# Performance work log

Measured on AMD Instinct MI355X. Metric: run time of the kernel, lower is better.

Reference implementation:

```python
import jax, jax.numpy as jnp
import numpy as np


def setup_inputs() -> dict:
    key = jax.random.key(0)
    kx, ky = jax.random.split(key)
    B, Sx, Sy, D = 8, 2048, 2048, 128
    x = jax.random.normal(kx, (B, Sx, D), dtype=jnp.float32)
    y = jax.random.normal(ky, (B, Sy, D), dtype=jnp.float32)
    return {"x": x, "y": y}


def reference(x, y):
    # score[b, i, j] = softmax_j(x[b,i,:] . y[b,j,:])
    score = jax.nn.softmax(jnp.einsum("bid,bjd->bij", x, y), axis=-1)
    # dropout is identity in eval mode (reference baseline)
    att_map = jnp.einsum("bij,bjd->bid", score, y)
    return x + att_map
```

## Files before the change

kernel.cpp:

```cpp
#include <hip/hip_runtime.h>
#include <hip/hip_fp16.h>


#define SX 2048
#define SY 2048
#define DD 128
#define KVBLK 64
#define NWAVE 8
#define QBLK (NWAVE * 32)
#define NTHREADS (NWAVE * 64)
#define L2E 1.4426950408889634f
#define RTHR 4.0f

typedef __attribute__((ext_vector_type(8))) _Float16 f16x8;
typedef __attribute__((ext_vector_type(4))) _Float16 f16x4;
typedef __attribute__((ext_vector_type(4))) float f32x4;
typedef __attribute__((ext_vector_type(16))) float f32x16;
typedef __attribute__((ext_vector_type(4))) unsigned int u32x4;

template<bool WRITEB>
__global__ __launch_bounds__(256) void prepass(const float* __restrict__ y,
                                               _Float16* __restrict__ yB,
                                               _Float16* __restrict__ yT)
{
    __shared__ _Float16 T[64 * 64];
    char* Tb = (char*)T;
    const int tid = (int)threadIdx.x;
    const int b = blockIdx.y;
    const int k0 = (blockIdx.x >> 1) * 64;
    const int d0 = (blockIdx.x & 1) * 64;
    const float* yb = y + (size_t)b * SY * DD;
#pragma unroll
    for (int t = 0; t < 2; ++t) {
        int cid = t * 256 + tid;
        int row = cid >> 3, c = cid & 7;
        const float* gp = yb + (size_t)(k0 + row) * DD + d0 + c * 8;
        f32x4 a0 = *(const f32x4*)gp;
        f32x4 a1 = *(const f32x4*)(gp + 4);
        f16x8 v;
#pragma unroll
        for (int j = 0; j < 4; ++j) { v[j] = (_Float16)a0[j]; v[4 + j] = (_Float16)a1[j]; }
        if constexpr (WRITEB)
            *(f16x8*)(yB + ((size_t)b * SY + k0 + row) * DD + d0 + c * 8) = v;
        *(f16x8*)(Tb + ((row * 128 + c * 16) ^ ((row & 7) << 4))) = v;
    }
    __syncthreads();
#pragma unroll
    for (int t = 0; t < 2; ++t) {
        int cid = t * 256 + tid;
        int drow = cid >> 3, ck = cid & 7;
        f16x8 v;
#pragma unroll
        for (int j = 0; j < 8; ++j)
            v[j] = *(const _Float16*)(Tb + ((((ck * 8 + j) * 128) + drow * 2) ^ (j << 4)));
        *(f16x8*)(yT + ((size_t)b * DD + d0 + drow) * SY + k0 + ck * 8) = v;
    }
}

template<bool SPLITOUT, int MODE>
__global__ __launch_bounds__(NTHREADS) void attn_fwd(
    const float* __restrict__ xg, const float* __restrict__ yg,
    const _Float16* __restrict__ yB, const _Float16* __restrict__ yT,
    float* __restrict__ og, _Float16* __restrict__ Opart,
    float* __restrict__ mpart, float* __restrict__ lpart,
    int kv_len, int nb)
{
    __shared__ __align__(16) unsigned char smem[2][32768];

    const int tid = (int)threadIdx.x;
    const int lane = tid & 63;
    const int wv = tid >> 6;
    const int l31 = lane & 31;
    const int hi = lane >> 5;
    const int swz = (l31 & 7) << 4;
    const int b = blockIdx.y;
    const int qbase = blockIdx.x * QBLK;
    const int sp = blockIdx.z;
    const int kv_begin = sp * kv_len;
    const int nt = kv_len / KVBLK;

    const float* xb = xg + (size_t)b * SX * DD;
    const float* yb = yg + (size_t)b * SY * DD;

    const int qrow = qbase + wv * 32 + l31;
    f16x8 qreg[8];
#pragma unroll
    for (int kst = 0; kst < 8; ++kst) {
        const float* qp = xb + (size_t)qrow * DD + kst * 16 + hi * 8;
        f32x4 q0 = *(const f32x4*)qp;
        f32x4 q1 = *(const f32x4*)(qp + 4);
        f16x8 v;
#pragma unroll
        for (int j = 0; j < 4; ++j) { v[j] = (_Float16)q0[j]; v[4 + j] = (_Float16)q1[j]; }
        qreg[kst] = v;
    }

    f16x8 kh[2];
    f32x4 kf[4];
    f16x8 vh[2];

    auto LOADT = [&](int kv0) {
#pragma unroll
        for (int c = 0; c < 2; ++c) {
            int cid = c * NTHREADS + tid;
            int krow = cid >> 4, kc8 = cid & 15;
            if constexpr (MODE == 2) {
                kh[c] = *(const f16x8*)(yB + ((size_t)b * SY + kv0 + krow) * DD + kc8 * 8);
            } else {
                const float* gp = yb + (size_t)(kv0 + krow) * DD + kc8 * 8;
                kf[c * 2]     = *(const f32x4*)gp;
                kf[c * 2 + 1] = *(const f32x4*)(gp + 4);
            }
        }
        if constexpr (MODE >= 1) {
#pragma unroll
            for (int c = 0; c < 2; ++c) {
                int cid = c * NTHREADS + tid;
                int d = cid >> 3, kc = cid & 7;
                vh[c] = *(const f16x8*)(yT + ((size_t)b * DD + d) * SY + kv0 + kc * 8);
            }
        }
    };
    auto STORET = [&](char* Kb, char* Vb) {
#pragma unroll
        for (int c = 0; c < 2; ++c) {
            int cid = c * NTHREADS + tid;
            int krow = cid >> 4, kc8 = cid & 15;
            f16x8 kv;
            if constexpr (MODE == 2) {
                kv = kh[c];
            } else {
#pragma unroll
                for (int j = 0; j < 4; ++j) { kv[j] = (_Float16)kf[c * 2][j]; kv[4 + j] = (_Float16)kf[c * 2 + 1][j]; }
            }
            *(f16x8*)(Kb + ((krow * 256 + kc8 * 16) ^ ((krow & 7) << 4))) = kv;
            if constexpr (MODE == 0) {
#pragma unroll
                for (int j = 0; j < 8; ++j) {
                    int d = kc8 * 8 + j;
                    *(_Float16*)(Vb + ((d * 128 + krow * 2) ^ ((d & 7) << 4))) = kv[j];
                }
            }
        }
        if constexpr (MODE >= 1) {
#pragma unroll
            for (int c = 0; c < 2; ++c) {
                int cid = c * NTHREADS + tid;
                int d = cid >> 3, kc = cid & 7;
                *(f16x8*)(Vb + ((d * 128 + kc * 16) ^ ((d & 7) << 4))) = vh[c];
            }
        }
    };

    f32x16 o[4];
#pragma unroll
    for (int dt = 0; dt < 4; ++dt) o[dt] = f32x16{};
    float m = -3.0e38f, ls = 0.f;

    LOADT(kv_begin);
    STORET((char*)smem[0], (char*)smem[0] + 16384);
    __syncthreads();

    for (int t = 0; t < nt; ++t) {
        char* Kb = (char*)smem[t & 1];
        char* Vb = Kb + 16384;
        if (t + 1 < nt) LOADT(kv_begin + (t + 1) * KVBLK);

        f32x16 sc[2];
        __builtin_amdgcn_s_setprio(1);
#pragma unroll
        for (int s = 0; s < 2; ++s) {
            f32x16 acc = f32x16{};
#pragma unroll
            for (int kst = 0; kst < 8; ++kst) {
                f16x8 kfr = *(const f16x8*)(Kb + (((32 * s + l31) * 256 + kst * 32 + hi * 16) ^ swz));
                acc = __builtin_amdgcn_mfma_f32_32x32x16_f16(kfr, qreg[kst], acc, 0, 0, 0);
            }
            sc[s] = acc;
        }
        __builtin_amdgcn_s_setprio(0);

        float tv[16];
#pragma unroll
        for (int r = 0; r < 16; ++r) tv[r] = fmaxf(sc[0][r], sc[1][r]);
#pragma unroll
        for (int st = 8; st >= 1; st >>= 1)
#pragma unroll
            for (int i = 0; i < 8; ++i)
                if (i < st) tv[i] = fmaxf(tv[i], tv[i + st]);
        float tm = tv[0];
        tm = fmaxf(tm, __shfl_xor(tm, 32, 64));
        if (!__all(tm <= m + RTHR)) {
            float mn = fmaxf(m, tm);
            float al = __builtin_exp2f((m - mn) * L2E);
            m = mn;
            ls *= al;
#pragma unroll
            for (int dt = 0; dt < 4; ++dt)
#pragma unroll
                for (int r = 0; r < 16; ++r) o[dt][r] *= al;
        }
        float mnl = m * L2E;

        float gsum[4];
#pragma unroll
        for (int s = 0; s < 2; ++s) {
#pragma unroll
            for (int k = 0; k < 2; ++k) {
                float p0 = __builtin_exp2f(__builtin_fmaf(sc[s][8 * k + 0], L2E, -mnl));
                float p1 = __builtin_exp2f(__builtin_fmaf(sc[s][8 * k + 1], L2E, -mnl));
                float p2 = __builtin_exp2f(__builtin_fmaf(sc[s][8 * k + 2], L2E, -mnl));
                float p3 = __builtin_exp2f(__builtin_fmaf(sc[s][8 * k + 3], L2E, -mnl));
                float p4 = __builtin_exp2f(__builtin_fmaf(sc[s][8 * k + 4], L2E, -mnl));
                float p5 = __builtin_exp2f(__builtin_fmaf(sc[s][8 * k + 5], L2E, -mnl));
                float p6 = __builtin_exp2f(__builtin_fmaf(sc[s][8 * k + 6], L2E, -mnl));
                float p7 = __builtin_exp2f(__builtin_fmaf(sc[s][8 * k + 7], L2E, -mnl));
                gsum[s * 2 + k] = ((p0 + p1) + (p2 + p3)) + ((p4 + p5) + (p6 + p7));
                unsigned aw = __builtin_bit_cast(unsigned, __builtin_amdgcn_cvt_pkrtz(p0, p1));
                unsigned cw = __builtin_bit_cast(unsigned, __builtin_amdgcn_cvt_pkrtz(p2, p3));
                unsigned bw = __builtin_bit_cast(unsigned, __builtin_amdgcn_cvt_pkrtz(p4, p5));
                unsigned dw = __builtin_bit_cast(unsigned, __builtin_amdgcn_cvt_pkrtz(p6, p7));
                asm("v_permlane32_swap_b32 %0, %1" : "+v"(aw), "+v"(bw));
                asm("v_permlane32_swap_b32 %0, %1" : "+v"(cw), "+v"(dw));
                u32x4 ww;
                ww[0] = aw;
                ww[1] = cw;
                ww[2] = bw;
                ww[3] = dw;
                f16x8 pf = __builtin_bit_cast(f16x8, ww);
                __builtin_amdgcn_s_setprio(1);
#pragma unroll
                for (int dt = 0; dt < 4; ++dt) {
                    f16x8 vf = *(const f16x8*)(Vb + (((dt * 32 + l31) * 128 + 64 * s + 32 * k + 16 * hi) ^ swz));
                    o[dt] = __builtin_amdgcn_mfma_f32_32x32x16_f16(vf, pf, o[dt], 0, 0, 0);
                }
                __builtin_amdgcn_s_setprio(0);
            }
        }
        float ps = (gsum[0] + gsum[1]) + (gsum[2] + gsum[3]);
        ps += __shfl_xor(ps, 32, 64);
        ls += ps;

        if (t + 1 < nt) {
            char* Kn = (char*)smem[(t + 1) & 1];
            STORET(Kn, Kn + 16384);
        }
        __syncthreads();
    }

    float inv = SPLITOUT ? 1.0f : (1.0f / ls);
    if constexpr (SPLITOUT) {
        if (lane < 32) {
            size_t mi = ((size_t)sp * nb + b) * SX + qrow;
            mpart[mi] = m;
            lpart[mi] = ls;
        }
    }
    char* Ep = (char*)smem[0] + wv * 4096;
    for (int dt = 0; dt < 4; ++dt) {
#pragma unroll
        for (int g = 0; g < 4; ++g)
#pragma unroll
            for (int t4 = 0; t4 < 4; ++t4) {
                int r = g * 4 + t4;
                int dl = t4 + 8 * g + 4 * hi;
                *(float*)(Ep + (l31 * 128 + ((dl * 4) ^ swz))) = o[dt][r] * inv;
            }
        asm volatile("s_waitcnt lgkmcnt(0)" ::: "memory");
        if constexpr (SPLITOUT) {
            _Float16* Ob = Opart + ((size_t)sp * nb + b) * SX * DD;
#pragma unroll
            for (int i = 0; i < 2; ++i) {
                int id = i * 64 + lane;
                int q2 = id >> 2, c8 = id & 3;
                int qs = (q2 & 7) << 4;
                f32x4 e0 = *(const f32x4*)(Ep + (q2 * 128 + ((c8 * 32) ^ qs)));
                f32x4 e1 = *(const f32x4*)(Ep + (q2 * 128 + ((c8 * 32 + 16) ^ qs)));
                f16x8 h;
#pragma unroll
                for (int j = 0; j < 4; ++j) { h[j] = (_Float16)e0[j]; h[4 + j] = (_Float16)e1[j]; }
                *(f16x8*)(Ob + (size_t)(qbase + wv * 32 + q2) * DD + dt * 32 + c8 * 8) = h;
            }
        } else {
            float* ob = og + (size_t)b * SX * DD;
#pragma unroll
            for (int i = 0; i < 4; ++i) {
                int id = i * 64 + lane;
                int q2 = id >> 3, ch = id & 7;
                int qs = (q2 & 7) << 4;
                f32x4 e = *(const f32x4*)(Ep + (q2 * 128 + ((ch * 16) ^ qs)));
                size_t gi = (size_t)(qbase + wv * 32 + q2) * DD + dt * 32 + ch * 4;
                f32x4 xv = *(const f32x4*)(xb + gi);
                f32x4 rs;
#pragma unroll
                for (int j = 0; j < 4; ++j) rs[j] = xv[j] + e[j];
                *(f32x4*)(ob + gi) = rs;
            }
        }
        asm volatile("s_waitcnt lgkmcnt(0)" ::: "memory");
    }
}

__global__ __launch_bounds__(256) void combine(const float* __restrict__ x,
    const _Float16* __restrict__ Opart, const float* __restrict__ mpart,
    const float* __restrict__ lpart, float* __restrict__ out, int nb, int nsplit)
{
    int tid = (int)threadIdx.x;
    int gr = blockIdx.x * 8 + (tid >> 5);
    int c = tid & 31;
    size_t nrows = (size_t)nb * SX;
    float M = -3.0e38f;
    for (int s = 0; s < nsplit; ++s) M = fmaxf(M, mpart[(size_t)s * nrows + gr]);
    float wsum = 0.f;
    float acc[4] = {0.f, 0.f, 0.f, 0.f};
    for (int s = 0; s < nsplit; ++s) {
        float ms = mpart[(size_t)s * nrows + gr];
        float lv = lpart[(size_t)s * nrows + gr];
        float wv = __builtin_exp2f((ms - M) * L2E);
        wsum += wv * lv;
        f16x4 h = *(const f16x4*)(Opart + (size_t)s * nrows * DD + (size_t)gr * DD + c * 4);
#pragma unroll
        for (int j = 0; j < 4; ++j) acc[j] += wv * (float)h[j];
    }
    float inv = 1.0f / wsum;
    size_t off = (size_t)gr * DD + c * 4;
    f32x4 xv = *(const f32x4*)(x + off);
    f32x4 rs;
#pragma unroll
    for (int j = 0; j < 4; ++j) rs[j] = xv[j] + acc[j] * inv;
    *(f32x4*)(out + off) = rs;
}

extern "C" void kernel_launch(void* const* d_in, const int* in_sizes, int n_in,
                              void* d_out, int out_size, void* d_ws, size_t ws_size,
                              hipStream_t stream) {
    const float* x = (const float*)d_in[0];
    const float* y = (const float*)d_in[1];
    float* out = (float*)d_out;
    int nb = in_sizes[0] / (SX * DD);

    size_t yBsz = (size_t)nb * SY * DD * sizeof(_Float16);
    size_t yTsz = yBsz;
    auto opsz = [&](int n) { return (size_t)n * nb * SX * DD * sizeof(_Float16); };
    auto mlsz = [&](int n) { return (size_t)n * nb * SX * sizeof(float); };
    char* w = (char*)d_ws;
    dim3 pgrid((SY / 64) * (DD / 64), nb);

    if (ws_size >= yBsz + yTsz + opsz(4) + 2 * mlsz(4)) {
        _Float16* yB = (_Float16*)w;
        _Float16* yT = (_Float16*)(w + yBsz);
        _Float16* Op = (_Float16*)(w + yBsz + yTsz);
        float* mp = (float*)(w + yBsz + yTsz + opsz(4));
        float* lp = mp + (size_t)4 * nb * SX;
        prepass<true><<<pgrid, 256, 0, stream>>>(y, yB, yT);
        attn_fwd<true, 2><<<dim3(SX / QBLK, nb, 4), NTHREADS, 0, stream>>>(
            x, y, yB, yT, out, Op, mp, lp, SY / 4, nb);
        combine<<<dim3(nb * SX / 8), 256, 0, stream>>>(x, Op, mp, lp, out, nb, 4);
    } else if (ws_size >= yTsz + opsz(4) + 2 * mlsz(4)) {
        _Float16* yT = (_Float16*)w;
        _Float16* Op = (_Float16*)(w + yTsz);
        float* mp = (float*)(w + yTsz + opsz(4));
        float* lp = mp + (size_t)4 * nb * SX;
        prepass<false><<<pgrid, 256, 0, stream>>>(y, nullptr, yT);
        attn_fwd<true, 1><<<dim3(SX / QBLK, nb, 4), NTHREADS, 0, stream>>>(
            x, y, nullptr, yT, out, Op, mp, lp, SY / 4, nb);
        combine<<<dim3(nb * SX / 8), 256, 0, stream>>>(x, Op, mp, lp, out, nb, 4);
    } else if (ws_size >= yTsz + opsz(2) + 2 * mlsz(2)) {
        _Float16* yT = (_Float16*)w;
        _Float16* Op = (_Float16*)(w + yTsz);
        float* mp = (float*)(w + yTsz + opsz(2));
        float* lp = mp + (size_t)2 * nb * SX;
        prepass<false><<<pgrid, 256, 0, stream>>>(y, nullptr, yT);
        attn_fwd<true, 1><<<dim3(SX / QBLK, nb, 2), NTHREADS, 0, stream>>>(
            x, y, nullptr, yT, out, Op, mp, lp, SY / 2, nb);
        combine<<<dim3(nb * SX / 8), 256, 0, stream>>>(x, Op, mp, lp, out, nb, 2);
    } else if (ws_size >= yTsz) {
        _Float16* yT = (_Float16*)w;
        prepass<false><<<pgrid, 256, 0, stream>>>(y, nullptr, yT);
        attn_fwd<false, 1><<<dim3(SX / QBLK, nb, 1), NTHREADS, 0, stream>>>(
            x, y, nullptr, yT, out, nullptr, nullptr, nullptr, SY, nb);
    } else {
        attn_fwd<false, 0><<<dim3(SX / QBLK, nb, 1), NTHREADS, 0, stream>>>(
            x, y, nullptr, nullptr, out, nullptr, nullptr, nullptr, SY, nb);
    }
}
```

Baseline: 48.15 us.

## Add 16-wave, 8-way KV-split attention path with templated wave count

New measurement: 125.7 us. 2.61x slower.

```diff
diff --git a/kernel.cpp b/kernel.cpp
--- a/kernel.cpp
+++ b/kernel.cpp
@@ -6,9 +6,6 @@
 #define SY 2048
 #define DD 128
 #define KVBLK 64
-#define NWAVE 8
-#define QBLK (NWAVE * 32)
-#define NTHREADS (NWAVE * 64)
 #define L2E 1.4426950408889634f
 #define RTHR 4.0f
 
@@ -57,14 +54,18 @@
     }
 }
 
-template<bool SPLITOUT, int MODE>
-__global__ __launch_bounds__(NTHREADS) void attn_fwd(
+template<bool SPLITOUT, int MODE, int NW>
+__global__ __launch_bounds__(NW * 64, (NW >= 16) ? 4 : 2) void attn_fwd(
     const float* __restrict__ xg, const float* __restrict__ yg,
     const _Float16* __restrict__ yB, const _Float16* __restrict__ yT,
     float* __restrict__ og, _Float16* __restrict__ Opart,
     float* __restrict__ mpart, float* __restrict__ lpart,
     int kv_len, int nb)
 {
+    constexpr int NTH = NW * 64;
+    constexpr int QB = NW * 32;
+    constexpr int NCHK = (KVBLK * DD * 2) / (NTH * 16);
+
     __shared__ __align__(16) unsigned char smem[2][32768];
 
     const int tid = (int)threadIdx.x;
@@ -74,7 +75,7 @@
     const int hi = lane >> 5;
     const int swz = (l31 & 7) << 4;
     const int b = blockIdx.y;
-    const int qbase = blockIdx.x * QBLK;
+    const int qbase = blockIdx.x * QB;
     const int sp = blockIdx.z;
     const int kv_begin = sp * kv_len;
     const int nt = kv_len / KVBLK;
@@ -95,14 +96,14 @@
         qreg[kst] = v;
     }
 
-    f16x8 kh[2];
-    f32x4 kf[4];
-    f16x8 vh[2];
+    f16x8 kh[NCHK];
+    f32x4 kf[2 * NCHK];
+    f16x8 vh[NCHK];
 
     auto LOADT = [&](int kv0) {
 #pragma unroll
-        for (int c = 0; c < 2; ++c) {
-            int cid = c * NTHREADS + tid;
+        for (int c = 0; c < NCHK; ++c) {
+            int cid = c * NTH + tid;
             int krow = cid >> 4, kc8 = cid & 15;
             if constexpr (MODE == 2) {
                 kh[c] = *(const f16x8*)(yB + ((size_t)b * SY + kv0 + krow) * DD + kc8 * 8);
@@ -112,19 +113,17 @@
                 kf[c * 2 + 1] = *(const f32x4*)(gp + 4);
             }
         }
-        if constexpr (MODE >= 1) {
-#pragma unroll
-            for (int c = 0; c < 2; ++c) {
-                int cid = c * NTHREADS + tid;
-                int d = cid >> 3, kc = cid & 7;
-                vh[c] = *(const f16x8*)(yT + ((size_t)b * DD + d) * SY + kv0 + kc * 8);
-            }
+#pragma unroll
+        for (int c = 0; c < NCHK; ++c) {
+            int cid = c * NTH + tid;
+            int d = cid >> 3, kc = cid & 7;
+            vh[c] = *(const f16x8*)(yT + ((size_t)b * DD + d) * SY + kv0 + kc * 8);
         }
     };
     auto STORET = [&](char* Kb, char* Vb) {
 #pragma unroll
-        for (int c = 0; c < 2; ++c) {
-            int cid = c * NTHREADS + tid;
+        for (int c = 0; c < NCHK; ++c) {
+            int cid = c * NTH + tid;
             int krow = cid >> 4, kc8 = cid & 15;
             f16x8 kv;
             if constexpr (MODE == 2) {
@@ -134,21 +133,12 @@
                 for (int j = 0; j < 4; ++j) { kv[j] = (_Float16)kf[c * 2][j]; kv[4 + j] = (_Float16)kf[c * 2 + 1][j]; }
             }
             *(f16x8*)(Kb + ((krow * 256 + kc8 * 16) ^ ((krow & 7) << 4))) = kv;
-            if constexpr (MODE == 0) {
-#pragma unroll
-                for (int j = 0; j < 8; ++j) {
-                    int d = kc8 * 8 + j;
-                    *(_Float16*)(Vb + ((d * 128 + krow * 2) ^ ((d & 7) << 4))) = kv[j];
-                }
-            }
-        }
-        if constexpr (MODE >= 1) {
-#pragma unroll
-            for (int c = 0; c < 2; ++c) {
-                int cid = c * NTHREADS + tid;
-                int d = cid >> 3, kc = cid & 7;
-                *(f16x8*)(Vb + ((d * 128 + kc * 16) ^ ((d & 7) << 4))) = vh[c];
-            }
+        }
+#pragma unroll
+        for (int c = 0; c < NCHK; ++c) {
+            int cid = c * NTH + tid;
+            int d = cid >> 3, kc = cid & 7;
+            *(f16x8*)(Vb + ((d * 128 + kc * 16) ^ ((d & 7) << 4))) = vh[c];
         }
     };
 
@@ -346,14 +336,24 @@
     char* w = (char*)d_ws;
     dim3 pgrid((SY / 64) * (DD / 64), nb);
 
-    if (ws_size >= yBsz + yTsz + opsz(4) + 2 * mlsz(4)) {
+    if (ws_size >= yBsz + yTsz + opsz(8) + 2 * mlsz(8)) {
+        _Float16* yB = (_Float16*)w;
+        _Float16* yT = (_Float16*)(w + yBsz);
+        _Float16* Op = (_Float16*)(w + yBsz + yTsz);
+        float* mp = (float*)(w + yBsz + yTsz + opsz(8));
+        float* lp = mp + (size_t)8 * nb * SX;
+        prepass<true><<<pgrid, 256, 0, stream>>>(y, yB, yT);
+        attn_fwd<true, 2, 16><<<dim3(SX / 512, nb, 8), 1024, 0, stream>>>(
+            x, y, yB, yT, out, Op, mp, lp, SY / 8, nb);
+        combine<<<dim3(nb * SX / 8), 256, 0, stream>>>(x, Op, mp, lp, out, nb, 8);
+    } else if (ws_size >= yBsz + yTsz + opsz(4) + 2 * mlsz(4)) {
         _Float16* yB = (_Float16*)w;
         _Float16* yT = (_Float16*)(w + yBsz);
         _Float16* Op = (_Float16*)(w + yBsz + yTsz);
         float* mp = (float*)(w + yBsz + yTsz + opsz(4));
         float* lp = mp + (size_t)4 * nb * SX;
         prepass<true><<<pgrid, 256, 0, stream>>>(y, yB, yT);
-        attn_fwd<true, 2><<<dim3(SX / QBLK, nb, 4), NTHREADS, 0, stream>>>(
+        attn_fwd<true, 2, 8><<<dim3(SX / 256, nb, 4), 512, 0, stream>>>(
             x, y, yB, yT, out, Op, mp, lp, SY / 4, nb);
         combine<<<dim3(nb * SX / 8), 256, 0, stream>>>(x, Op, mp, lp, out, nb, 4);
     } else if (ws_size >= yTsz + opsz(4) + 2 * mlsz(4)) {
@@ -362,25 +362,13 @@
         float* mp = (float*)(w + yTsz + opsz(4));
         float* lp = mp + (size_t)4 * nb * SX;
         prepass<false><<<pgrid, 256, 0, stream>>>(y, nullptr, yT);
-        attn_fwd<true, 1><<<dim3(SX / QBLK, nb, 4), NTHREADS, 0, stream>>>(
+        attn_fwd<true, 1, 8><<<dim3(SX / 256, nb, 4), 512, 0, stream>>>(
             x, y, nullptr, yT, out, Op, mp, lp, SY / 4, nb);
         combine<<<dim3(nb * SX / 8), 256, 0, stream>>>(x, Op, mp, lp, out, nb, 4);
-    } else if (ws_size >= yTsz + opsz(2) + 2 * mlsz(2)) {
-        _Float16* yT = (_Float16*)w;
-        _Float16* Op = (_Float16*)(w + yTsz);
-        float* mp = (float*)(w + yTsz + opsz(2));
-        float* lp = mp + (size_t)2 * nb * SX;
-        prepass<false><<<pgrid, 256, 0, stream>>>(y, nullptr, yT);
-        attn_fwd<true, 1><<<dim3(SX / QBLK, nb, 2), NTHREADS, 0, stream>>>(
-            x, y, nullptr, yT, out, Op, mp, lp, SY / 2, nb);
-        combine<<<dim3(nb * SX / 8), 256, 0, stream>>>(x, Op, mp, lp, out, nb, 2);
-    } else if (ws_size >= yTsz) {
+    } else {
         _Float16* yT = (_Float16*)w;
         prepass<false><<<pgrid, 256, 0, stream>>>(y, nullptr, yT);
-        attn_fwd<false, 1><<<dim3(SX / QBLK, nb, 1), NTHREADS, 0, stream>>>(
+        attn_fwd<false, 1, 8><<<dim3(SX / 256, nb, 1), 512, 0, stream>>>(
             x, y, nullptr, yT, out, nullptr, nullptr, nullptr, SY, nb);
-    } else {
-        attn_fwd<false, 0><<<dim3(SX / QBLK, nb, 1), NTHREADS, 0, stream>>>(
-            x, y, nullptr, nullptr, out, nullptr, nullptr, nullptr, SY, nb);
     }
 }
```

## Software-pipeline QK^T of next tile with softmax/PV of previous tile, triple-buffer LDS

Applied to the files above, without the earlier changes.

Result: slower. 49.94 us (+3.7%).

```diff
diff --git a/kernel.cpp b/kernel.cpp
--- a/kernel.cpp
+++ b/kernel.cpp
@@ -65,7 +65,7 @@
     float* __restrict__ mpart, float* __restrict__ lpart,
     int kv_len, int nb)
 {
-    __shared__ __align__(16) unsigned char smem[2][32768];
+    __shared__ __align__(16) unsigned char smem[3][32768];
 
     const int tid = (int)threadIdx.x;
     const int lane = tid & 63;
@@ -159,93 +159,103 @@
 
     LOADT(kv_begin);
     STORET((char*)smem[0], (char*)smem[0] + 16384);
+    if (nt > 1) LOADT(kv_begin + KVBLK);
     __syncthreads();
 
-    for (int t = 0; t < nt; ++t) {
-        char* Kb = (char*)smem[t & 1];
-        char* Vb = Kb + 16384;
-        if (t + 1 < nt) LOADT(kv_begin + (t + 1) * KVBLK);
-
-        f32x16 sc[2];
-        __builtin_amdgcn_s_setprio(1);
-#pragma unroll
-        for (int s = 0; s < 2; ++s) {
-            f32x16 acc = f32x16{};
-#pragma unroll
-            for (int kst = 0; kst < 8; ++kst) {
-                f16x8 kfr = *(const f16x8*)(Kb + (((32 * s + l31) * 256 + kst * 32 + hi * 16) ^ swz));
-                acc = __builtin_amdgcn_mfma_f32_32x32x16_f16(kfr, qreg[kst], acc, 0, 0, 0);
-            }
-            sc[s] = acc;
-        }
-        __builtin_amdgcn_s_setprio(0);
-
-        float tv[16];
-#pragma unroll
-        for (int r = 0; r < 16; ++r) tv[r] = fmaxf(sc[0][r], sc[1][r]);
-#pragma unroll
-        for (int st = 8; st >= 1; st >>= 1)
-#pragma unroll
-            for (int i = 0; i < 8; ++i)
-                if (i < st) tv[i] = fmaxf(tv[i], tv[i + st]);
-        float tm = tv[0];
-        tm = fmaxf(tm, __shfl_xor(tm, 32, 64));
-        if (!__all(tm <= m + RTHR)) {
-            float mn = fmaxf(m, tm);
-            float al = __builtin_exp2f((m - mn) * L2E);
-            m = mn;
-            ls *= al;
-#pragma unroll
-            for (int dt = 0; dt < 4; ++dt)
-#pragma unroll
-                for (int r = 0; r < 16; ++r) o[dt][r] *= al;
-        }
-        float mnl = m * L2E;
-
-        float gsum[4];
-#pragma unroll
-        for (int s = 0; s < 2; ++s) {
-#pragma unroll
-            for (int k = 0; k < 2; ++k) {
-                float p0 = __builtin_exp2f(__builtin_fmaf(sc[s][8 * k + 0], L2E, -mnl));
-                float p1 = __builtin_exp2f(__builtin_fmaf(sc[s][8 * k + 1], L2E, -mnl));
-                float p2 = __builtin_exp2f(__builtin_fmaf(sc[s][8 * k + 2], L2E, -mnl));
-                float p3 = __builtin_exp2f(__builtin_fmaf(sc[s][8 * k + 3], L2E, -mnl));
-                float p4 = __builtin_exp2f(__builtin_fmaf(sc[s][8 * k + 4], L2E, -mnl));
-                float p5 = __builtin_exp2f(__builtin_fmaf(sc[s][8 * k + 5], L2E, -mnl));
-                float p6 = __builtin_exp2f(__builtin_fmaf(sc[s][8 * k + 6], L2E, -mnl));
-                float p7 = __builtin_exp2f(__builtin_fmaf(sc[s][8 * k + 7], L2E, -mnl));
-                gsum[s * 2 + k] = ((p0 + p1) + (p2 + p3)) + ((p4 + p5) + (p6 + p7));
-                unsigned aw = __builtin_bit_cast(unsigned, __builtin_amdgcn_cvt_pkrtz(p0, p1));
-                unsigned cw = __builtin_bit_cast(unsigned, __builtin_amdgcn_cvt_pkrtz(p2, p3));
-                unsigned bw = __builtin_bit_cast(unsigned, __builtin_amdgcn_cvt_pkrtz(p4, p5));
-                unsigned dw = __builtin_bit_cast(unsigned, __builtin_amdgcn_cvt_pkrtz(p6, p7));
-                asm("v_permlane32_swap_b32 %0, %1" : "+v"(aw), "+v"(bw));
-                asm("v_permlane32_swap_b32 %0, %1" : "+v"(cw), "+v"(dw));
-                u32x4 ww;
-                ww[0] = aw;
-                ww[1] = cw;
-                ww[2] = bw;
-                ww[3] = dw;
-                f16x8 pf = __builtin_bit_cast(f16x8, ww);
-                __builtin_amdgcn_s_setprio(1);
-#pragma unroll
-                for (int dt = 0; dt < 4; ++dt) {
-                    f16x8 vf = *(const f16x8*)(Vb + (((dt * 32 + l31) * 128 + 64 * s + 32 * k + 16 * hi) ^ swz));
-                    o[dt] = __builtin_amdgcn_mfma_f32_32x32x16_f16(vf, pf, o[dt], 0, 0, 0);
+    f32x16 scA[2];
+    for (int t = 0; t <= nt; ++t) {
+        f32x16 scB[2];
+
+        if (t < nt) {
+            char* Kb = (char*)smem[t % 3];
+            __builtin_amdgcn_s_setprio(1);
+#pragma unroll
+            for (int s = 0; s < 2; ++s) {
+                f32x16 acc = f32x16{};
+#pragma unroll
+                for (int kst = 0; kst < 8; ++kst) {
+                    f16x8 kfr = *(const f16x8*)(Kb + (((32 * s + l31) * 256 + kst * 32 + hi * 16) ^ swz));
+                    acc = __builtin_amdgcn_mfma_f32_32x32x16_f16(kfr, qreg[kst], acc, 0, 0, 0);
                 }
-                __builtin_amdgcn_s_setprio(0);
-            }
-        }
-        float ps = (gsum[0] + gsum[1]) + (gsum[2] + gsum[3]);
-        ps += __shfl_xor(ps, 32, 64);
-        ls += ps;
+                scB[s] = acc;
+            }
+            __builtin_amdgcn_s_setprio(0);
+        }
+
+        if (t > 0) {
+            char* Vb = (char*)smem[(t - 1) % 3] + 16384;
+
+            float tv[16];
+#pragma unroll
+            for (int r = 0; r < 16; ++r) tv[r] = fmaxf(scA[0][r], scA[1][r]);
+#pragma unroll
+            for (int st = 8; st >= 1; st >>= 1)
+#pragma unroll
+                for (int i = 0; i < 8; ++i)
+                    if (i < st) tv[i] = fmaxf(tv[i], tv[i + st]);
+            float tm = tv[0];
+            tm = fmaxf(tm, __shfl_xor(tm, 32, 64));
+            if (!__all(tm <= m + RTHR)) {
+                float mn = fmaxf(m, tm);
+                float al = __builtin_exp2f((m - mn) * L2E);
+                m = mn;
+                ls *= al;
+#pragma unroll
+                for (int dt = 0; dt < 4; ++dt)
+#pragma unroll
+                    for (int r = 0; r < 16; ++r) o[dt][r] *= al;
+            }
+            float mnl = m * L2E;
+
+            float gsum[4];
+#pragma unroll
+            for (int s = 0; s < 2; ++s) {
+#pragma unroll
+                for (int k = 0; k < 2; ++k) {
+                    float p0 = __builtin_exp2f(__builtin_fmaf(scA[s][8 * k + 0], L2E, -mnl));
+                    float p1 = __builtin_exp2f(__builtin_fmaf(scA[s][8 * k + 1], L2E, -mnl));
+                    float p2 = __builtin_exp2f(__builtin_fmaf(scA[s][8 * k + 2], L2E, -mnl));
+                    float p3 = __builtin_exp2f(__builtin_fmaf(scA[s][8 * k + 3], L2E, -mnl));
+                    float p4 = __builtin_exp2f(__builtin_fmaf(scA[s][8 * k + 4], L2E, -mnl));
+                    float p5 = __builtin_exp2f(__builtin_fmaf(scA[s][8 * k + 5], L2E, -mnl));
+                    float p6 = __builtin_exp2f(__builtin_fmaf(scA[s][8 * k + 6], L2E, -mnl));
+                    float p7 = __builtin_exp2f(__builtin_fmaf(scA[s][8 * k + 7], L2E, -mnl));
+                    gsum[s * 2 + k] = ((p0 + p1) + (p2 + p3)) + ((p4 + p5) + (p6 + p7));
+                    unsigned aw = __builtin_bit_cast(unsigned, __builtin_amdgcn_cvt_pkrtz(p0, p1));
+                    unsigned cw = __builtin_bit_cast(unsigned, __builtin_amdgcn_cvt_pkrtz(p2, p3));
+                    unsigned bw = __builtin_bit_cast(unsigned, __builtin_amdgcn_cvt_pkrtz(p4, p5));
+                    unsigned dw = __builtin_bit_cast(unsigned, __builtin_amdgcn_cvt_pkrtz(p6, p7));
+                    asm("v_permlane32_swap_b32 %0, %1" : "+v"(aw), "+v"(bw));
+                    asm("v_permlane32_swap_b32 %0, %1" : "+v"(cw), "+v"(dw));
+                    u32x4 ww;
+                    ww[0] = aw;
+                    ww[1] = cw;
+                    ww[2] = bw;
+                    ww[3] = dw;
+                    f16x8 pf = __builtin_bit_cast(f16x8, ww);
+                    __builtin_amdgcn_s_setprio(1);
+#pragma unroll
+                    for (int dt = 0; dt < 4; ++dt) {
+                        f16x8 vf = *(const f16x8*)(Vb + (((dt * 32 + l31) * 128 + 64 * s + 32 * k + 16 * hi) ^ swz));
+                        o[dt] = __builtin_amdgcn_mfma_f32_32x32x16_f16(vf, pf, o[dt], 0, 0, 0);
+                    }
+                    __builtin_amdgcn_s_setprio(0);
+                }
+            }
+            float ps = (gsum[0] + gsum[1]) + (gsum[2] + gsum[3]);
+            ps += __shfl_xor(ps, 32, 64);
+            ls += ps;
+        }
 
         if (t + 1 < nt) {
-            char* Kn = (char*)smem[(t + 1) & 1];
+            char* Kn = (char*)smem[(t + 1) % 3];
             STORET(Kn, Kn + 16384);
         }
+        if (t + 2 < nt) LOADT(kv_begin + (t + 2) * KVBLK);
+
         __syncthreads();
+        scA[0] = scB[0];
+        scA[1] = scB[1];
     }
 
     float inv = SPLITOUT ? 1.0f : (1.0f / ls);
```
